# Kernel tuning notes

Measured on AMD Instinct MI355X. Metric: run time of the kernel, lower is better.

## Reference

```python
import jax, jax.numpy as jnp
import numpy as np

H = 16
D_MODEL = 1024
D_K = D_MODEL // H
SEQ = 4096


def setup_inputs() -> dict:
    key = jax.random.key(0)
    ks = jax.random.split(key, 11)
    s = 1.0 / np.sqrt(D_MODEL)
    inp = {
        "query": jax.random.normal(ks[0], (SEQ, D_MODEL), dtype=jnp.float32),
        "key": jax.random.normal(ks[1], (SEQ, D_MODEL), dtype=jnp.float32),
        "value": jax.random.normal(ks[2], (SEQ, D_MODEL), dtype=jnp.float32),
        "Wq": jax.random.uniform(ks[3], (D_MODEL, D_MODEL), jnp.float32, -s, s),
        "bq": jax.random.uniform(ks[4], (D_MODEL,), jnp.float32, -s, s),
        "Wk": jax.random.uniform(ks[5], (D_MODEL, D_MODEL), jnp.float32, -s, s),
        "bk": jax.random.uniform(ks[6], (D_MODEL,), jnp.float32, -s, s),
        "Wv": jax.random.uniform(ks[7], (D_MODEL, D_MODEL), jnp.float32, -s, s),
        "bv": jax.random.uniform(ks[8], (D_MODEL,), jnp.float32, -s, s),
        "Wo": jax.random.uniform(ks[9], (D_MODEL, D_MODEL), jnp.float32, -s, s),
        "bo": jax.random.uniform(ks[10], (D_MODEL,), jnp.float32, -s, s),
    }
    return inp


def reference(query, key, value, Wq, bq, Wk, bk, Wv, bv, Wo, bo):
    # Linear projections (torch Linear: x @ W.T + b), then split heads.
    # [S, d_model] -> [S, h, d_k] -> [h, S, d_k]
    def proj(x, W, b):
        return (x @ W.T + b).reshape(-1, H, D_K).transpose(1, 0, 2)

    q = proj(query, Wq, bq)   # [h, S, d_k]
    k = proj(key, Wk, bk)     # [h, S, d_k]
    v = proj(value, Wv, bv)   # [h, S, d_k]

    scale = 1.0 / jnp.sqrt(jnp.asarray(D_K, dtype=q.dtype))
    scores = jnp.einsum("hnd,hmd->hnm", q, k) * scale  # [h, S, S]
    p_attn = jax.nn.softmax(scores, axis=-1)
    x = jnp.einsum("hnm,hmd->hnd", p_attn, v)           # [h, S, d_k]
    x = x.transpose(1, 0, 2).reshape(-1, H * D_K)        # [S, d_model]
    return x @ Wo.T + bo
```

## Files before the change

### kernel.cpp

```cpp
#include <hip/hip_runtime.h>
#include <hip/hip_bf16.h>
#include <stdint.h>

#define HN     16
#define DMODEL 1024
#define DKH    64
#define SEQL   4096

typedef __attribute__((ext_vector_type(8))) short bf16x8;
typedef __attribute__((ext_vector_type(4))) float f32x4;

typedef const __attribute__((address_space(1))) uint32_t gas_u32;
typedef __attribute__((address_space(3))) uint32_t las_u32;

__device__ __forceinline__ void gl_lds16(const void* g, void* l) {
  __builtin_amdgcn_global_load_lds((gas_u32*)g, (las_u32*)l, 16, 0, 0);
}

__device__ __forceinline__ unsigned short f2bf(float x) {
  uint32_t u = __float_as_uint(x);
  u = (u + 0x7fffu + ((u >> 16) & 1u)) >> 16;
  return (unsigned short)u;
}

__device__ __forceinline__ uint32_t cvt_pk_bf16(float lo, float hi) {
  uint32_t r;
  asm("v_cvt_pk_bf16_f32 %0, %1, %2" : "=v"(r) : "v"(lo), "v"(hi));
  return r;
}

__device__ __forceinline__ float fast_exp2(float x) {
  float r;
  asm("v_exp_f32 %0, %1" : "=v"(r) : "v"(x));
  return r;
}

struct CvtArgs {
  const float *q, *k, *v, *wq, *wk, *wv, *wo;
  unsigned short *qb, *kb, *vb, *wqb, *wkb, *wvb, *wob;
};

__global__ __launch_bounds__(256) void cvt_all(CvtArgs a) {
  const int stride = gridDim.x * blockDim.x;
  for (int v4 = blockIdx.x * blockDim.x + threadIdx.x; v4 < 4194304; v4 += stride) {
    const float* sp; unsigned short* dp; int idx;
    if      (v4 < 1048576) { sp = a.q;  dp = a.qb;  idx = v4; }
    else if (v4 < 2097152) { sp = a.k;  dp = a.kb;  idx = v4 - 1048576; }
    else if (v4 < 3145728) { sp = a.v;  dp = a.vb;  idx = v4 - 2097152; }
    else if (v4 < 3407872) { sp = a.wq; dp = a.wqb; idx = v4 - 3145728; }
    else if (v4 < 3670016) { sp = a.wk; dp = a.wkb; idx = v4 - 3407872; }
    else if (v4 < 3932160) { sp = a.wv; dp = a.wvb; idx = v4 - 3670016; }
    else                   { sp = a.wo; dp = a.wob; idx = v4 - 3932160; }
    float4 f = ((const float4*)sp)[idx];
    ushort4 o;
    o.x = f2bf(f.x); o.y = f2bf(f.y); o.z = f2bf(f.z); o.w = f2bf(f.w);
    ((ushort4*)dp)[idx] = o;
  }
}

struct GemmDesc {
  const unsigned short* A;
  const unsigned short* W;
  const float* bias;
  void* C;
  int mode;
  float scale;
};
struct GemmArgs { GemmDesc d[3]; };

__global__ __launch_bounds__(256) void gemm_bt(GemmArgs ga) {
  const GemmDesc gd = ga.d[blockIdx.z];
  constexpr int M = SEQL, N = DMODEL, K = DMODEL;
  __shared__ unsigned short As[128 * 64];
  __shared__ unsigned short Bs[128 * 64];
  const int tid = threadIdx.x;
  const int w = tid >> 6, lane = tid & 63;
  const int g16 = lane >> 4, l16 = lane & 15;
  const int wr = w >> 1, wc = w & 1;
  const int bm0 = blockIdx.y * 128, bn0 = blockIdx.x * 128;
  const int srow = tid >> 3, scc = tid & 7;

  f32x4 acc[4][4];
#pragma unroll
  for (int i = 0; i < 4; ++i)
#pragma unroll
    for (int j = 0; j < 4; ++j)
      acc[i][j] = (f32x4){0.f, 0.f, 0.f, 0.f};

  for (int k0 = 0; k0 < K; k0 += 64) {
#pragma unroll
    for (int i = 0; i < 4; ++i) {
      int row = i * 32 + srow;
      int sw = scc ^ (row & 7);
      gl_lds16(gd.A + (size_t)(bm0 + row) * K + k0 + sw * 8,
               (void*)(As + (i * 256 + w * 64) * 8));
      gl_lds16(gd.W + (size_t)(bn0 + row) * K + k0 + sw * 8,
               (void*)(Bs + (i * 256 + w * 64) * 8));
    }
    __syncthreads();
#pragma unroll
    for (int ks = 0; ks < 2; ++ks) {
      bf16x8 af[4], bfr[4];
#pragma unroll
      for (int mt = 0; mt < 4; ++mt) {
        int row = wr * 64 + mt * 16 + l16;
        af[mt] = *(const bf16x8*)&As[row * 64 + (((ks * 4 + g16) ^ (row & 7)) * 8)];
      }
#pragma unroll
      for (int nt = 0; nt < 4; ++nt) {
        int row = wc * 64 + nt * 16 + l16;
        bfr[nt] = *(const bf16x8*)&Bs[row * 64 + (((ks * 4 + g16) ^ (row & 7)) * 8)];
      }
#pragma unroll
      for (int mt = 0; mt < 4; ++mt)
#pragma unroll
        for (int nt = 0; nt < 4; ++nt)
          acc[mt][nt] = __builtin_amdgcn_mfma_f32_16x16x32_bf16(af[mt], bfr[nt], acc[mt][nt], 0, 0, 0);
    }
    __syncthreads();
  }

#pragma unroll
  for (int nt = 0; nt < 4; ++nt) {
    int col = bn0 + wc * 64 + nt * 16 + l16;
    float bcol = gd.bias[col];
#pragma unroll
    for (int mt = 0; mt < 4; ++mt) {
      int row0 = bm0 + wr * 64 + mt * 16 + g16 * 4;
      f32x4 a = acc[mt][nt];
      if (gd.mode == 0) {
        unsigned short* CB = (unsigned short*)gd.C;
#pragma unroll
        for (int r = 0; r < 4; ++r)
          CB[(size_t)(row0 + r) * N + col] = f2bf((a[r] + bcol) * gd.scale);
      } else if (gd.mode == 1) {
        unsigned short* CT = (unsigned short*)gd.C;
        ushort4 pk;
        pk.x = f2bf(a[0] + bcol); pk.y = f2bf(a[1] + bcol);
        pk.z = f2bf(a[2] + bcol); pk.w = f2bf(a[3] + bcol);
        *(ushort4*)&CT[(size_t)col * M + row0] = pk;
      } else {
        float* CF = (float*)gd.C;
#pragma unroll
        for (int r = 0; r < 4; ++r)
          CF[(size_t)(row0 + r) * N + col] = a[r] + bcol;
      }
    }
  }
}

__global__ __launch_bounds__(256, 3) void attn_fwd(
    const unsigned short* __restrict__ Qm, const unsigned short* __restrict__ Km,
    const unsigned short* __restrict__ Vtm, unsigned short* __restrict__ Xm) {
  __shared__ __align__(16) unsigned short Ksm[2 * 4096];
  __shared__ __align__(16) unsigned short Vsm[2 * 4096];
  __shared__ __align__(16) unsigned short Psm[4096];
  const int tid = threadIdx.x;
  const int w = tid >> 6, lane = tid & 63;
  const int g = lane >> 4, qi = lane & 15;
  const int hb = blockIdx.y * DKH;
  const int q0 = blockIdx.x * 64 + w * 16;
  const int srow = tid >> 3, scc = tid & 7;
  const float THR = 12.0f;

  const int r0 = srow, r1 = 32 + srow;
  const unsigned short* kp0 = Km + (size_t)r0 * DMODEL + hb + (scc ^ (r0 & 7)) * 8;
  const unsigned short* kp1 = Km + (size_t)r1 * DMODEL + hb + (scc ^ (r1 & 7)) * 8;
  const unsigned short* vp0 = Vtm + (size_t)(hb + r0) * SEQL + (scc ^ (r0 & 7)) * 8;
  const unsigned short* vp1 = Vtm + (size_t)(hb + r1) * SEQL + (scc ^ (r1 & 7)) * 8;
  unsigned short* kd0 = Ksm + (w * 64) * 8;
  unsigned short* kd1 = Ksm + (256 + w * 64) * 8;
  unsigned short* vd0 = Vsm + (w * 64) * 8;
  unsigned short* vd1 = Vsm + (256 + w * 64) * 8;

  const unsigned short* kb0 = &Ksm[qi * 64 + (((0 + g) ^ (qi & 7)) * 8)];
  const unsigned short* kb1 = &Ksm[qi * 64 + (((4 + g) ^ (qi & 7)) * 8)];
  const unsigned short* vrb0 = &Vsm[qi * 64 + (((0 + g) ^ (qi & 7)) * 8)];
  const unsigned short* vrb1 = &Vsm[qi * 64 + (((4 + g) ^ (qi & 7)) * 8)];

  int pw0 = w * 1024 + qi * 64 + (((0 + (g >> 1)) ^ (qi & 7)) * 8) + (g & 1) * 4;
  int pw1 = w * 1024 + qi * 64 + (((2 + (g >> 1)) ^ (qi & 7)) * 8) + (g & 1) * 4;
  int pw2 = w * 1024 + qi * 64 + (((4 + (g >> 1)) ^ (qi & 7)) * 8) + (g & 1) * 4;
  int pw3 = w * 1024 + qi * 64 + (((6 + (g >> 1)) ^ (qi & 7)) * 8) + (g & 1) * 4;
  const unsigned short* prb0 = &Psm[w * 1024 + qi * 64 + (((0 + g) ^ (qi & 7)) * 8)];
  const unsigned short* prb1 = &Psm[w * 1024 + qi * 64 + (((4 + g) ^ (qi & 7)) * 8)];

  union { uint32_t u[4]; bf16x8 v; } onef;
  onef.u[0] = onef.u[1] = onef.u[2] = onef.u[3] = 0x3F803F80u;

  bf16x8 qf[2];
#pragma unroll
  for (int ks = 0; ks < 2; ++ks)
    qf[ks] = *(const bf16x8*)&Qm[(size_t)(q0 + qi) * DMODEL + hb + ks * 32 + g * 8];

  f32x4 oacc[4];
#pragma unroll
  for (int i = 0; i < 4; ++i) oacc[i] = (f32x4){0.f, 0.f, 0.f, 0.f};
  f32x4 lacc = (f32x4){0.f, 0.f, 0.f, 0.f};
  float mrun = -1e30f;

  gl_lds16(kp0, kd0); gl_lds16(kp1, kd1);
  gl_lds16(vp0, vd0); gl_lds16(vp1, vd1);
  kp0 += 64 * DMODEL; kp1 += 64 * DMODEL; vp0 += 64; vp1 += 64;
  asm volatile("s_waitcnt vmcnt(0)" ::: "memory");
  __builtin_amdgcn_s_barrier();

#define ATTN_STEP(BUF)                                                         \
  do {                                                                         \
       \
    gl_lds16(kp0, kd0 + ((BUF) ^ 1) * 4096);                                   \
    gl_lds16(kp1, kd1 + ((BUF) ^ 1) * 4096);                                   \
    gl_lds16(vp0, vd0 + ((BUF) ^ 1) * 4096);                                   \
    gl_lds16(vp1, vd1 + ((BUF) ^ 1) * 4096);                                   \
    kp0 += 64 * DMODEL; kp1 += 64 * DMODEL; vp0 += 64; vp1 += 64;              \
    f32x4 sv[4];                                                               \
    _Pragma("unroll")                                                          \
    for (int kvt = 0; kvt < 4; ++kvt) sv[kvt] = (f32x4){0.f, 0.f, 0.f, 0.f};   \
    __builtin_amdgcn_s_setprio(1);                                             \
    _Pragma("unroll")                                                          \
    for (int kvt = 0; kvt < 4; ++kvt) {                                        \
      bf16x8 ka0 = *(const bf16x8*)(kb0 + (BUF) * 4096 + kvt * 1024);          \
      bf16x8 ka1 = *(const bf16x8*)(kb1 + (BUF) * 4096 + kvt * 1024);          \
      sv[kvt] = __builtin_amdgcn_mfma_f32_16x16x32_bf16(ka0, qf[0], sv[kvt], 0, 0, 0); \
      sv[kvt] = __builtin_amdgcn_mfma_f32_16x16x32_bf16(ka1, qf[1], sv[kvt], 0, 0, 0); \
    }                                                                          \
    __builtin_amdgcn_s_setprio(0);                                             \
    float tmax = sv[0][0];                                                     \
    _Pragma("unroll")                                                          \
    for (int kvt = 0; kvt < 4; ++kvt)                                          \
      _Pragma("unroll")                                                        \
      for (int r = 0; r < 4; ++r) tmax = fmaxf(tmax, sv[kvt][r]);              \
    tmax = fmaxf(tmax, __shfl_xor(tmax, 16));                                  \
    tmax = fmaxf(tmax, __shfl_xor(tmax, 32));                                  \
    if (__any(tmax - mrun > THR)) {                                            \
      float mnew = fmaxf(mrun, tmax);                                          \
      float alpha = fast_exp2(mrun - mnew);                                    \
      _Pragma("unroll")                                                        \
      for (int r = 0; r < 4; ++r) {                                            \
        float ar = __shfl(alpha, (lane & 48) + g * 4 + r);                     \
        lacc[r] *= ar;                                                         \
        _Pragma("unroll")                                                      \
        for (int dg = 0; dg < 4; ++dg) oacc[dg][r] *= ar;                      \
      }                                                                        \
      mrun = mnew;                                                             \
    }                                                                          \
    float p[16];                                                               \
    _Pragma("unroll")                                                          \
    for (int kvt = 0; kvt < 4; ++kvt)                                          \
      _Pragma("unroll")                                                        \
      for (int r = 0; r < 4; ++r)                                              \
        p[kvt * 4 + r] = fast_exp2(sv[kvt][r] - mrun);                         \
    uint2 pk;                                                                  \
    pk.x = cvt_pk_bf16(p[0], p[1]);  pk.y = cvt_pk_bf16(p[2], p[3]);           \
    *(uint2*)&Psm[pw0] = pk;                                                   \
    pk.x = cvt_pk_bf16(p[4], p[5]);  pk.y = cvt_pk_bf16(p[6], p[7]);           \
    *(uint2*)&Psm[pw1] = pk;                                                   \
    pk.x = cvt_pk_bf16(p[8], p[9]);  pk.y = cvt_pk_bf16(p[10], p[11]);         \
    *(uint2*)&Psm[pw2] = pk;                                                   \
    pk.x = cvt_pk_bf16(p[12], p[13]); pk.y = cvt_pk_bf16(p[14], p[15]);        \
    *(uint2*)&Psm[pw3] = pk;                                                   \
    bf16x8 pa0 = *(const bf16x8*)prb0;                                         \
    bf16x8 pa1 = *(const bf16x8*)prb1;                                         \
    __builtin_amdgcn_s_setprio(1);                                             \
    lacc = __builtin_amdgcn_mfma_f32_16x16x32_bf16(pa0, onef.v, lacc, 0, 0, 0);\
    lacc = __builtin_amdgcn_mfma_f32_16x16x32_bf16(pa1, onef.v, lacc, 0, 0, 0);\
    _Pragma("unroll")                                                          \
    for (int dg = 0; dg < 4; ++dg) {                                           \
      bf16x8 vb0 = *(const bf16x8*)(vrb0 + (BUF) * 4096 + dg * 1024);          \
      bf16x8 vb1 = *(const bf16x8*)(vrb1 + (BUF) * 4096 + dg * 1024);          \
      oacc[dg] = __builtin_amdgcn_mfma_f32_16x16x32_bf16(pa0, vb0, oacc[dg], 0, 0, 0); \
      oacc[dg] = __builtin_amdgcn_mfma_f32_16x16x32_bf16(pa1, vb1, oacc[dg], 0, 0, 0); \
    }                                                                          \
    __builtin_amdgcn_s_setprio(0);                                             \
    asm volatile("s_waitcnt vmcnt(0)" ::: "memory");                           \
    __builtin_amdgcn_s_barrier();                                              \
  } while (0)

  for (int tt = 0; tt < SEQL / 128; ++tt) {
    ATTN_STEP(0);
    ATTN_STEP(1);
  }
#undef ATTN_STEP

#pragma unroll
  for (int r = 0; r < 4; ++r) {
    float inv = 1.f / lacc[r];
    int row = q0 + g * 4 + r;
#pragma unroll
    for (int dg = 0; dg < 4; ++dg)
      Xm[(size_t)row * DMODEL + hb + dg * 16 + qi] = f2bf(oacc[dg][r] * inv);
  }
}

extern "C" void kernel_launch(void* const* d_in, const int* in_sizes, int n_in,
                              void* d_out, int out_size, void* d_ws, size_t ws_size,
                              hipStream_t stream) {
  const float* query = (const float*)d_in[0];
  const float* key_  = (const float*)d_in[1];
  const float* value = (const float*)d_in[2];
  const float* Wq = (const float*)d_in[3];
  const float* bq = (const float*)d_in[4];
  const float* Wk = (const float*)d_in[5];
  const float* bk = (const float*)d_in[6];
  const float* Wv = (const float*)d_in[7];
  const float* bv = (const float*)d_in[8];
  const float* Wo = (const float*)d_in[9];
  const float* bo = (const float*)d_in[10];

  char* ws = (char*)d_ws;
  const size_t MB = 1024 * 1024;
  unsigned short* qb  = (unsigned short*)(ws + 0 * MB);
  unsigned short* kb  = (unsigned short*)(ws + 8 * MB);
  unsigned short* vb  = (unsigned short*)(ws + 16 * MB);
  unsigned short* wqb = (unsigned short*)(ws + 24 * MB);
  unsigned short* wkb = (unsigned short*)(ws + 26 * MB);
  unsigned short* wvb = (unsigned short*)(ws + 28 * MB);
  unsigned short* wob = (unsigned short*)(ws + 30 * MB);
  unsigned short* Qp  = (unsigned short*)(ws + 32 * MB);
  unsigned short* Kp  = (unsigned short*)(ws + 40 * MB);
  unsigned short* Vtp = (unsigned short*)(ws + 48 * MB);
  unsigned short* Xp  = (unsigned short*)(ws + 56 * MB);

  CvtArgs ca{query, key_, value, Wq, Wk, Wv, Wo, qb, kb, vb, wqb, wkb, wvb, wob};
  cvt_all<<<dim3(2048), dim3(256), 0, stream>>>(ca);

  const float CE = 0.18033688011112042f;
  GemmArgs gp;
  gp.d[0] = GemmDesc{qb, wqb, bq, (void*)Qp, 0, CE};
  gp.d[1] = GemmDesc{kb, wkb, bk, (void*)Kp, 0, 1.0f};
  gp.d[2] = GemmDesc{vb, wvb, bv, (void*)Vtp, 1, 1.0f};
  gemm_bt<<<dim3(8, 32, 3), dim3(256), 0, stream>>>(gp);

  attn_fwd<<<dim3(SEQL / 64, HN), dim3(256), 0, stream>>>(Qp, Kp, Vtp, Xp);

  GemmArgs go;
  go.d[0] = GemmDesc{Xp, wob, bo, d_out, 2, 1.0f};
  go.d[1] = go.d[0];
  go.d[2] = go.d[0];
  gemm_bt<<<dim3(8, 32, 1), dim3(256), 0, stream>>>(go);
}
```

Baseline: 290.6 us.

## Process two query tiles per wave in attention; add dedicated output-projection GEMM

```diff
diff --git a/kernel.cpp b/kernel.cpp
--- a/kernel.cpp
+++ b/kernel.cpp
@@ -133,18 +133,85 @@
 #pragma unroll
         for (int r = 0; r < 4; ++r)
           CB[(size_t)(row0 + r) * N + col] = f2bf((a[r] + bcol) * gd.scale);
-      } else if (gd.mode == 1) {
+      } else {
         unsigned short* CT = (unsigned short*)gd.C;
         ushort4 pk;
         pk.x = f2bf(a[0] + bcol); pk.y = f2bf(a[1] + bcol);
         pk.z = f2bf(a[2] + bcol); pk.w = f2bf(a[3] + bcol);
         *(ushort4*)&CT[(size_t)col * M + row0] = pk;
-      } else {
-        float* CF = (float*)gd.C;
-#pragma unroll
-        for (int r = 0; r < 4; ++r)
-          CF[(size_t)(row0 + r) * N + col] = a[r] + bcol;
       }
+    }
+  }
+}
+
+__global__ __launch_bounds__(256) void gemm_o(
+    const unsigned short* __restrict__ A, const unsigned short* __restrict__ W,
+    const float* __restrict__ bias, float* __restrict__ C) {
+  constexpr int N = DMODEL, K = DMODEL;
+  __shared__ unsigned short As[128 * 64];
+  __shared__ unsigned short Bs[64 * 64];
+  const int tid = threadIdx.x;
+  const int w = tid >> 6, lane = tid & 63;
+  const int g16 = lane >> 4, l16 = lane & 15;
+  const int wr = w >> 1, wc = w & 1;
+  const int bm0 = blockIdx.y * 128, bn0 = blockIdx.x * 64;
+  const int srow = tid >> 3, scc = tid & 7;
+
+  f32x4 acc[4][2];
+#pragma unroll
+  for (int i = 0; i < 4; ++i)
+#pragma unroll
+    for (int j = 0; j < 2; ++j)
+      acc[i][j] = (f32x4){0.f, 0.f, 0.f, 0.f};
+
+  for (int k0 = 0; k0 < K; k0 += 64) {
+#pragma unroll
+    for (int i = 0; i < 4; ++i) {
+      int row = i * 32 + srow;
+      int sw = scc ^ (row & 7);
+      gl_lds16(A + (size_t)(bm0 + row) * K + k0 + sw * 8,
+               (void*)(As + (i * 256 + w * 64) * 8));
+    }
+#pragma unroll
+    for (int i = 0; i < 2; ++i) {
+      int row = i * 32 + srow;
+      int sw = scc ^ (row & 7);
+      gl_lds16(W + (size_t)(bn0 + row) * K + k0 + sw * 8,
+               (void*)(Bs + (i * 256 + w * 64) * 8));
+    }
+    __syncthreads();
+#pragma unroll
+    for (int ks = 0; ks < 2; ++ks) {
+      bf16x8 af[4], bfr[2];
+#pragma unroll
+      for (int mt = 0; mt < 4; ++mt) {
+        int row = wr * 64 + mt * 16 + l16;
+        af[mt] = *(const bf16x8*)&As[row * 64 + (((ks * 4 + g16) ^ (row & 7)) * 8)];
+      }
+#pragma unroll
+      for (int nt = 0; nt < 2; ++nt) {
+        int row = wc * 32 + nt * 16 + l16;
+        bfr[nt] = *(const bf16x8*)&Bs[row * 64 + (((ks * 4 + g16) ^ (row & 7)) * 8)];
+      }
+#pragma unroll
+      for (int mt = 0; mt < 4; ++mt)
+#pragma unroll
+        for (int nt = 0; nt < 2; ++nt)
+          acc[mt][nt] = __builtin_amdgcn_mfma_f32_16x16x32_bf16(af[mt], bfr[nt], acc[mt][nt], 0, 0, 0);
+    }
+    __syncthreads();
+  }
+
+#pragma unroll
+  for (int nt = 0; nt < 2; ++nt) {
+    int col = bn0 + wc * 32 + nt * 16 + l16;
+    float bcol = bias[col];
+#pragma unroll
+    for (int mt = 0; mt < 4; ++mt) {
+      int row0 = bm0 + wr * 64 + mt * 16 + g16 * 4;
+#pragma unroll
+      for (int r = 0; r < 4; ++r)
+        C[(size_t)(row0 + r) * N + col] = acc[mt][nt][r] + bcol;
     }
   }
 }
@@ -154,12 +221,12 @@
     const unsigned short* __restrict__ Vtm, unsigned short* __restrict__ Xm) {
   __shared__ __align__(16) unsigned short Ksm[2 * 4096];
   __shared__ __align__(16) unsigned short Vsm[2 * 4096];
-  __shared__ __align__(16) unsigned short Psm[4096];
+  __shared__ __align__(16) unsigned short Psm[8192];
   const int tid = threadIdx.x;
   const int w = tid >> 6, lane = tid & 63;
   const int g = lane >> 4, qi = lane & 15;
   const int hb = blockIdx.y * DKH;
-  const int q0 = blockIdx.x * 64 + w * 16;
+  const int q0 = blockIdx.x * 128 + w * 32;
   const int srow = tid >> 3, scc = tid & 7;
   const float THR = 12.0f;
 
@@ -178,26 +245,32 @@
   const unsigned short* vrb0 = &Vsm[qi * 64 + (((0 + g) ^ (qi & 7)) * 8)];
   const unsigned short* vrb1 = &Vsm[qi * 64 + (((4 + g) ^ (qi & 7)) * 8)];
 
-  int pw0 = w * 1024 + qi * 64 + (((0 + (g >> 1)) ^ (qi & 7)) * 8) + (g & 1) * 4;
-  int pw1 = w * 1024 + qi * 64 + (((2 + (g >> 1)) ^ (qi & 7)) * 8) + (g & 1) * 4;
-  int pw2 = w * 1024 + qi * 64 + (((4 + (g >> 1)) ^ (qi & 7)) * 8) + (g & 1) * 4;
-  int pw3 = w * 1024 + qi * 64 + (((6 + (g >> 1)) ^ (qi & 7)) * 8) + (g & 1) * 4;
-  const unsigned short* prb0 = &Psm[w * 1024 + qi * 64 + (((0 + g) ^ (qi & 7)) * 8)];
-  const unsigned short* prb1 = &Psm[w * 1024 + qi * 64 + (((4 + g) ^ (qi & 7)) * 8)];
+  const int pwb = w * 2048 + qi * 64 + (g & 1) * 4;
+  const int pw0 = pwb + (((0 + (g >> 1)) ^ (qi & 7)) * 8);
+  const int pw1 = pwb + (((2 + (g >> 1)) ^ (qi & 7)) * 8);
+  const int pw2 = pwb + (((4 + (g >> 1)) ^ (qi & 7)) * 8);
+  const int pw3 = pwb + (((6 + (g >> 1)) ^ (qi & 7)) * 8);
+  const unsigned short* prb0 = &Psm[w * 2048 + qi * 64 + (((0 + g) ^ (qi & 7)) * 8)];
+  const unsigned short* prb1 = &Psm[w * 2048 + qi * 64 + (((4 + g) ^ (qi & 7)) * 8)];
 
   union { uint32_t u[4]; bf16x8 v; } onef;
   onef.u[0] = onef.u[1] = onef.u[2] = onef.u[3] = 0x3F803F80u;
 
-  bf16x8 qf[2];
-#pragma unroll
-  for (int ks = 0; ks < 2; ++ks)
-    qf[ks] = *(const bf16x8*)&Qm[(size_t)(q0 + qi) * DMODEL + hb + ks * 32 + g * 8];
-
-  f32x4 oacc[4];
-#pragma unroll
-  for (int i = 0; i < 4; ++i) oacc[i] = (f32x4){0.f, 0.f, 0.f, 0.f};
-  f32x4 lacc = (f32x4){0.f, 0.f, 0.f, 0.f};
-  float mrun = -1e30f;
+  bf16x8 qf[2][2];
+#pragma unroll
+  for (int h = 0; h < 2; ++h)
+#pragma unroll
+    for (int ks = 0; ks < 2; ++ks)
+      qf[h][ks] = *(const bf16x8*)&Qm[(size_t)(q0 + h * 16 + qi) * DMODEL + hb + ks * 32 + g * 8];
+
+  f32x4 oacc[2][4];
+#pragma unroll
+  for (int h = 0; h < 2; ++h)
+#pragma unroll
+    for (int i = 0; i < 4; ++i) oacc[h][i] = (f32x4){0.f, 0.f, 0.f, 0.f};
+  f32x4 lacc[2];
+  lacc[0] = lacc[1] = (f32x4){0.f, 0.f, 0.f, 0.f};
+  float mrun[2] = {-1e30f, -1e30f};
 
   gl_lds16(kp0, kd0); gl_lds16(kp1, kd1);
   gl_lds16(vp0, vd0); gl_lds16(vp1, vd1);
@@ -207,69 +280,95 @@
 
 #define ATTN_STEP(BUF)                                                         \
   do {                                                                         \
-       \
     gl_lds16(kp0, kd0 + ((BUF) ^ 1) * 4096);                                   \
     gl_lds16(kp1, kd1 + ((BUF) ^ 1) * 4096);                                   \
     gl_lds16(vp0, vd0 + ((BUF) ^ 1) * 4096);                                   \
     gl_lds16(vp1, vd1 + ((BUF) ^ 1) * 4096);                                   \
     kp0 += 64 * DMODEL; kp1 += 64 * DMODEL; vp0 += 64; vp1 += 64;              \
-    f32x4 sv[4];                                                               \
-    _Pragma("unroll")                                                          \
-    for (int kvt = 0; kvt < 4; ++kvt) sv[kvt] = (f32x4){0.f, 0.f, 0.f, 0.f};   \
+    f32x4 sv[2][4];                                                            \
+    _Pragma("unroll")                                                          \
+    for (int h = 0; h < 2; ++h)                                                \
+      _Pragma("unroll")                                                        \
+      for (int kvt = 0; kvt < 4; ++kvt) sv[h][kvt] = (f32x4){0.f, 0.f, 0.f, 0.f}; \
     __builtin_amdgcn_s_setprio(1);                                             \
     _Pragma("unroll")                                                          \
     for (int kvt = 0; kvt < 4; ++kvt) {                                        \
       bf16x8 ka0 = *(const bf16x8*)(kb0 + (BUF) * 4096 + kvt * 1024);          \
       bf16x8 ka1 = *(const bf16x8*)(kb1 + (BUF) * 4096 + kvt * 1024);          \
-      sv[kvt] = __builtin_amdgcn_mfma_f32_16x16x32_bf16(ka0, qf[0], sv[kvt], 0, 0, 0); \
-      sv[kvt] = __builtin_amdgcn_mfma_f32_16x16x32_bf16(ka1, qf[1], sv[kvt], 0, 0, 0); \
+      _Pragma("unroll")                                                        \
+      for (int h = 0; h < 2; ++h) {                                            \
+        sv[h][kvt] = __builtin_amdgcn_mfma_f32_16x16x32_bf16(ka0, qf[h][0], sv[h][kvt], 0, 0, 0); \
+        sv[h][kvt] = __builtin_amdgcn_mfma_f32_16x16x32_bf16(ka1, qf[h][1], sv[h][kvt], 0, 0, 0); \
+      }                                                                        \
     }                                                                          \
     __builtin_amdgcn_s_setprio(0);                                             \
-    float tmax = sv[0][0];                                                     \
-    _Pragma("unroll")                                                          \
-    for (int kvt = 0; kvt < 4; ++kvt)                                          \
-      _Pragma("unroll")                                                        \
-      for (int r = 0; r < 4; ++r) tmax = fmaxf(tmax, sv[kvt][r]);              \
-    tmax = fmaxf(tmax, __shfl_xor(tmax, 16));                                  \
-    tmax = fmaxf(tmax, __shfl_xor(tmax, 32));                                  \
-    if (__any(tmax - mrun > THR)) {                                            \
-      float mnew = fmaxf(mrun, tmax);                                          \
-      float alpha = fast_exp2(mrun - mnew);                                    \
-      _Pragma("unroll")                                                        \
-      for (int r = 0; r < 4; ++r) {                                            \
-        float ar = __shfl(alpha, (lane & 48) + g * 4 + r);                     \
-        lacc[r] *= ar;                                                         \
+    float tmax[2];                                                             \
+    _Pragma("unroll")                                                          \
+    for (int h = 0; h < 2; ++h) {                                              \
+      float tm = sv[h][0][0];                                                  \
+      _Pragma("unroll")                                                        \
+      for (int kvt = 0; kvt < 4; ++kvt)                                        \
         _Pragma("unroll")                                                      \
-        for (int dg = 0; dg < 4; ++dg) oacc[dg][r] *= ar;                      \
+        for (int r = 0; r < 4; ++r) tm = fmaxf(tm, sv[h][kvt][r]);             \
+      tm = fmaxf(tm, __shfl_xor(tm, 16));                                      \
+      tm = fmaxf(tm, __shfl_xor(tm, 32));                                      \
+      tmax[h] = tm;                                                            \
+    }                                                                          \
+    float need = fmaxf(tmax[0] - mrun[0], tmax[1] - mrun[1]);                  \
+    if (__any(need > THR)) {                                                   \
+      _Pragma("unroll")                                                        \
+      for (int h = 0; h < 2; ++h) {                                            \
+        float mnew = fmaxf(mrun[h], tmax[h]);                                  \
+        float alpha = fast_exp2(mrun[h] - mnew);                               \
+        _Pragma("unroll")                                                      \
+        for (int r = 0; r < 4; ++r) {                                          \
+          float ar = __shfl(alpha, (lane & 48) + g * 4 + r);                   \
+          lacc[h][r] *= ar;                                                    \
+          _Pragma("unroll")                                                    \
+          for (int dg = 0; dg < 4; ++dg) oacc[h][dg][r] *= ar;                 \
+        }                                                                      \
+        mrun[h] = mnew;                                                        \
       }                                                                        \
-      mrun = mnew;                                                             \
-    }                                                                          \
-    float p[16];                                                               \
-    _Pragma("unroll")                                                          \
-    for (int kvt = 0; kvt < 4; ++kvt)                                          \
-      _Pragma("unroll")                                                        \
-      for (int r = 0; r < 4; ++r)                                              \
-        p[kvt * 4 + r] = fast_exp2(sv[kvt][r] - mrun);                         \
-    uint2 pk;                                                                  \
-    pk.x = cvt_pk_bf16(p[0], p[1]);  pk.y = cvt_pk_bf16(p[2], p[3]);           \
-    *(uint2*)&Psm[pw0] = pk;                                                   \
-    pk.x = cvt_pk_bf16(p[4], p[5]);  pk.y = cvt_pk_bf16(p[6], p[7]);           \
-    *(uint2*)&Psm[pw1] = pk;                                                   \
-    pk.x = cvt_pk_bf16(p[8], p[9]);  pk.y = cvt_pk_bf16(p[10], p[11]);         \
-    *(uint2*)&Psm[pw2] = pk;                                                   \
-    pk.x = cvt_pk_bf16(p[12], p[13]); pk.y = cvt_pk_bf16(p[14], p[15]);        \
-    *(uint2*)&Psm[pw3] = pk;                                                   \
-    bf16x8 pa0 = *(const bf16x8*)prb0;                                         \
-    bf16x8 pa1 = *(const bf16x8*)prb1;                                         \
+    }                                                                          \
+    _Pragma("unroll")                                                          \
+    for (int h = 0; h < 2; ++h) {                                              \
+      float p[16];                                                             \
+      _Pragma("unroll")                                                        \
+      for (int kvt = 0; kvt < 4; ++kvt)                                        \
+        _Pragma("unroll")                                                      \
+        for (int r = 0; r < 4; ++r)                                            \
+          p[kvt * 4 + r] = fast_exp2(sv[h][kvt][r] - mrun[h]);                 \
+      uint2 pk;                                                                \
+      pk.x = cvt_pk_bf16(p[0], p[1]);  pk.y = cvt_pk_bf16(p[2], p[3]);         \
+      *(uint2*)&Psm[pw0 + h * 1024] = pk;                                      \
+      pk.x = cvt_pk_bf16(p[4], p[5]);  pk.y = cvt_pk_bf16(p[6], p[7]);         \
+      *(uint2*)&Psm[pw1 + h * 1024] = pk;                                      \
+      pk.x = cvt_pk_bf16(p[8], p[9]);  pk.y = cvt_pk_bf16(p[10], p[11]);       \
+      *(uint2*)&Psm[pw2 + h * 1024] = pk;                                      \
+      pk.x = cvt_pk_bf16(p[12], p[13]); pk.y = cvt_pk_bf16(p[14], p[15]);      \
+      *(uint2*)&Psm[pw3 + h * 1024] = pk;                                      \
+    }                                                                          \
+    bf16x8 pa[2][2];                                                           \
+    _Pragma("unroll")                                                          \
+    for (int h = 0; h < 2; ++h) {                                              \
+      pa[h][0] = *(const bf16x8*)(prb0 + h * 1024);                            \
+      pa[h][1] = *(const bf16x8*)(prb1 + h * 1024);                            \
+    }                                                                          \
     __builtin_amdgcn_s_setprio(1);                                             \
-    lacc = __builtin_amdgcn_mfma_f32_16x16x32_bf16(pa0, onef.v, lacc, 0, 0, 0);\
-    lacc = __builtin_amdgcn_mfma_f32_16x16x32_bf16(pa1, onef.v, lacc, 0, 0, 0);\
+    _Pragma("unroll")                                                          \
+    for (int h = 0; h < 2; ++h) {                                              \
+      lacc[h] = __builtin_amdgcn_mfma_f32_16x16x32_bf16(pa[h][0], onef.v, lacc[h], 0, 0, 0); \
+      lacc[h] = __builtin_amdgcn_mfma_f32_16x16x32_bf16(pa[h][1], onef.v, lacc[h], 0, 0, 0); \
+    }                                                                          \
     _Pragma("unroll")                                                          \
     for (int dg = 0; dg < 4; ++dg) {                                           \
       bf16x8 vb0 = *(const bf16x8*)(vrb0 + (BUF) * 4096 + dg * 1024);          \
       bf16x8 vb1 = *(const bf16x8*)(vrb1 + (BUF) * 4096 + dg * 1024);          \
-      oacc[dg] = __builtin_amdgcn_mfma_f32_16x16x32_bf16(pa0, vb0, oacc[dg], 0, 0, 0); \
-      oacc[dg] = __builtin_amdgcn_mfma_f32_16x16x32_bf16(pa1, vb1, oacc[dg], 0, 0, 0); \
+      _Pragma("unroll")                                                        \
+      for (int h = 0; h < 2; ++h) {                                            \
+        oacc[h][dg] = __builtin_amdgcn_mfma_f32_16x16x32_bf16(pa[h][0], vb0, oacc[h][dg], 0, 0, 0); \
+        oacc[h][dg] = __builtin_amdgcn_mfma_f32_16x16x32_bf16(pa[h][1], vb1, oacc[h][dg], 0, 0, 0); \
+      }                                                                        \
     }                                                                          \
     __builtin_amdgcn_s_setprio(0);                                             \
     asm volatile("s_waitcnt vmcnt(0)" ::: "memory");                           \
@@ -283,13 +382,15 @@
 #undef ATTN_STEP
 
 #pragma unroll
-  for (int r = 0; r < 4; ++r) {
-    float inv = 1.f / lacc[r];
-    int row = q0 + g * 4 + r;
-#pragma unroll
-    for (int dg = 0; dg < 4; ++dg)
-      Xm[(size_t)row * DMODEL + hb + dg * 16 + qi] = f2bf(oacc[dg][r] * inv);
-  }
+  for (int h = 0; h < 2; ++h)
+#pragma unroll
+    for (int r = 0; r < 4; ++r) {
+      float inv = 1.f / lacc[h][r];
+      int row = q0 + h * 16 + g * 4 + r;
+#pragma unroll
+      for (int dg = 0; dg < 4; ++dg)
+        Xm[(size_t)row * DMODEL + hb + dg * 16 + qi] = f2bf(oacc[h][dg][r] * inv);
+    }
 }
 
 extern "C" void kernel_launch(void* const* d_in, const int* in_sizes, int n_in,
@@ -331,11 +432,7 @@
   gp.d[2] = GemmDesc{vb, wvb, bv, (void*)Vtp, 1, 1.0f};
   gemm_bt<<<dim3(8, 32, 3), dim3(256), 0, stream>>>(gp);
 
-  attn_fwd<<<dim3(SEQL / 64, HN), dim3(256), 0, stream>>>(Qp, Kp, Vtp, Xp);
-
-  GemmArgs go;
-  go.d[0] = GemmDesc{Xp, wob, bo, d_out, 2, 1.0f};
-  go.d[1] = go.d[0];
-  go.d[2] = go.d[0];
-  gemm_bt<<<dim3(8, 32, 1), dim3(256), 0, stream>>>(go);
-}
+  attn_fwd<<<dim3(SEQL / 128, HN), dim3(256), 0, stream>>>(Qp, Kp, Vtp, Xp);
+
+  gemm_o<<<dim3(16, 32), dim3(256), 0, stream>>>(Xp, wob, bo, (float*)d_out);
+}
```

New measurement: 280.1 us. -3.6%, faster.
